# Performance work log

Measured on AMD Instinct MI355X. Metric: run time of the kernel, lower is better.

## Reference

```python
import jax, jax.numpy as jnp
import numpy as np

# Module hyperparameters (from init_kwargs)
A, B, K, P, STRIDE, PAD, ITERS = 32, 32, 3, 4, 2, 0, 3
C = P * P          # 16, input pose matrix size
D = P * P          # 16, output pose matrix size
KK = K * K         # 9
KKA = KK * A       # 288
EPS = 1e-8


def setup_inputs() -> dict:
    key = jax.random.key(0)
    k1, k2 = jax.random.split(key)
    pose = jax.random.normal(k1, (4, A * C, 32, 32), dtype=jnp.float32)
    # kaiming-uniform-like scale for W [kkA, B*D, C]
    W = jax.random.normal(k2, (KKA, B * D, C), dtype=jnp.float32) / np.sqrt(C).astype(np.float32)
    return {"pose": pose, "W": W}


def _unfold(x):
    # Equivalent of F.unfold(x, K, stride=STRIDE, padding=0), channel-major,
    # kernel positions (ki, kj) fastest -> (b, ch, KK, l)
    b, ch, h, w = x.shape
    oh = (h - K) // STRIDE + 1
    ow = (w - K) // STRIDE + 1
    hi = STRIDE * (oh - 1) + 1
    wi = STRIDE * (ow - 1) + 1
    cols = [x[:, :, i:i + hi:STRIDE, j:j + wi:STRIDE]
            for i in range(K) for j in range(K)]
    p = jnp.stack(cols, axis=2)  # (b, ch, KK, oh, ow)
    return p.reshape(b, ch, KK, oh * ow), oh, ow


def _squash(s):
    # standard capsule squash along last (pose) dim
    n2 = jnp.sum(s * s, axis=-1, keepdims=True)
    return s * n2 / ((1.0 + n2) * jnp.sqrt(n2 + EPS))


def reference(pose, W):
    b = pose.shape[0]
    p, oh, ow = _unfold(pose)               # (b, A*C, KK, l)
    l = oh * ow
    # view(b,A,C,kk,l) -> permute(0,4,3,1,2) -> (b,l,kk,A,C) -> (b,l,kkA,C)
    p = p.reshape(b, A, C, KK, l).transpose(0, 4, 3, 1, 2).reshape(b, l, KKA, C)
    # votes: W [kkA, B*D, C] @ pose [..., C, 1]
    votes = jnp.einsum('kdc,blkc->blkd', W, p).reshape(b, l, KKA, B, D)
    # routing-by-agreement
    logits = jnp.zeros((b, l, KKA, B, 1), dtype=pose.dtype)
    v = None
    for _ in range(ITERS):
        c = jax.nn.softmax(logits, axis=3)              # over B output capsules
        s = jnp.sum(c * votes, axis=2, keepdims=True)   # (b, l, 1, B, D)
        v = _squash(s)
        logits = logits + jnp.sum(v * votes, axis=-1, keepdims=True)
    v = v[:, :, 0].reshape(b, l, B * D)     # (b, l, B*D)
    v = v.transpose(0, 2, 1)                # (b, B*D, l)
    return v.reshape(b, B * D, oh, ow)
```

## Files before the change

### kernel.cpp

```cpp
#include <hip/hip_runtime.h>
#include <math.h>

#define KC   18
#define KPC  16
#define NP   928
#define NPT  29

typedef __attribute__((ext_vector_type(8)))  short short8;
typedef __attribute__((ext_vector_type(16))) float f32x16;

__device__ __forceinline__ unsigned short f2bf(float x) {
    union { float f; unsigned u; } v; v.f = x;
    unsigned r = v.u + 0x7fffu + ((v.u >> 16) & 1u);
    return (unsigned short)(r >> 16);
}
__device__ __forceinline__ float bf2f(unsigned short h) {
    union { unsigned u; float f; } v; v.u = ((unsigned)h) << 16;
    return v.f;
}

__global__ void wprep(const float* __restrict__ W,
                      unsigned short* __restrict__ Whi,
                      unsigned short* __restrict__ Wlo)
{
    int idx = (blockIdx.x * 256 + threadIdx.x) * 4;
    float4 x = *(const float4*)(W + idx);
    ushort4 h, l;
    h.x = f2bf(x.x); l.x = f2bf(x.x - bf2f(h.x));
    h.y = f2bf(x.y); l.y = f2bf(x.y - bf2f(h.y));
    h.z = f2bf(x.z); l.z = f2bf(x.z - bf2f(h.z));
    h.w = f2bf(x.w); l.w = f2bf(x.w - bf2f(h.w));
    *(ushort4*)(Whi + idx) = h;
    *(ushort4*)(Wlo + idx) = l;
}

__global__ __launch_bounds__(256) void unfold(const float* __restrict__ pose,
                                              unsigned short* __restrict__ Phi,
                                              unsigned short* __restrict__ Plo)
{
    __shared__ float lds[16 * 1057];
    const int bid = blockIdx.x;
    const int batch = bid >> 5;
    const int a = bid & 31;
    const int t = threadIdx.x;

    const float* src = pose + ((size_t)batch * 512 + a * 16) * 1024;
#pragma unroll
    for (int c = 0; c < 16; ++c) {
        float4 v = *(const float4*)(src + c * 1024 + t * 4);
        float* d = &lds[c * 1057 + (t >> 3) * 33 + (t & 7) * 4];
        d[0] = v.x; d[1] = v.y; d[2] = v.z; d[3] = v.w;
    }
    __syncthreads();

    const int c = t & 15;
    const int px = t >> 4;
    for (int it = 0; it < 15; ++it) {
        int pos = it * 16 + px;
        bool ok = pos < 225;
        int pc = ok ? pos : 224;
        int oi = pc / 15, oj = pc - oi * 15;
#pragma unroll
        for (int ki = 0; ki < 3; ++ki)
#pragma unroll
            for (int kj = 0; kj < 3; ++kj) {
                float val = lds[c * 1057 + (oi * 2 + ki) * 33 + (oj * 2 + kj)];
                unsigned short hh = f2bf(val);
                unsigned short ll = f2bf(val - bf2f(hh));
                if (ok) {
                    size_t o = ((size_t)((ki * 3 + kj) * 32 + a) * NP
                                + batch * 225 + pos) * 16 + c;
                    Phi[o] = hh;
                    Plo[o] = ll;
                }
            }
    }
}

template<int ITER>
__global__ __launch_bounds__(512, 2) void route(const unsigned short* __restrict__ Whi,
                                                const unsigned short* __restrict__ Wlo,
                                                const unsigned short* __restrict__ Phi,
                                                const unsigned short* __restrict__ Plo,
                                                const float* __restrict__ V,
                                                unsigned short* __restrict__ part)
{
    __shared__ float2 smb[2][8][32];

    const int bid = blockIdx.x;
    const int pt = bid % NPT;
    const int kc = bid / NPT;
    const int t = threadIdx.x;
    const int w = t >> 6;
    const int l = t & 63;
    const int col = l & 31;
    const int h = l >> 5;
    const int gpos = pt * 32 + col;
    const int bd0 = w * 64;

    float vf[2][16];
    if constexpr (ITER > 0) {
        const float* vp = V + (size_t)gpos * 512 + bd0 + 4 * h;
#pragma unroll
        for (int m = 0; m < 2; ++m)
#pragma unroll
            for (int q = 0; q < 4; ++q) {
                float4 x = *(const float4*)(vp + m * 32 + 8 * q);
                vf[m][q * 4 + 0] = x.x; vf[m][q * 4 + 1] = x.y;
                vf[m][q * 4 + 2] = x.z; vf[m][q * 4 + 3] = x.w;
            }
    }

    f32x16 s[2];
#pragma unroll
    for (int m = 0; m < 2; ++m)
#pragma unroll
        for (int r = 0; r < 16; ++r) s[m][r] = 0.f;

    const size_t k0 = (size_t)kc * KPC;
    const unsigned short* pWh = Whi + (k0 * 512 + bd0 + col) * 16 + 8 * h;
    const unsigned short* pWl = Wlo + (k0 * 512 + bd0 + col) * 16 + 8 * h;
    const unsigned short* pPh = Phi + (k0 * NP + gpos) * 16 + 8 * h;
    const unsigned short* pPl = Plo + (k0 * NP + gpos) * 16 + 8 * h;

    short8 ah0 = *(const short8*)(pWh);
    short8 ah1 = *(const short8*)(pWh + 512);
    short8 al0 = *(const short8*)(pWl);
    short8 al1 = *(const short8*)(pWl + 512);
    short8 bh  = *(const short8*)(pPh);
    short8 bl  = *(const short8*)(pPl);

    for (int kl = 0; kl < KPC; ++kl) {
        const int nw = (kl + 1) * 8192;
        const int np = (kl + 1) * 14848;
        short8 nah0 = *(const short8*)(pWh + nw);
        short8 nah1 = *(const short8*)(pWh + nw + 512);
        short8 nal0 = *(const short8*)(pWl + nw);
        short8 nal1 = *(const short8*)(pWl + nw + 512);
        short8 nbh  = *(const short8*)(pPh + np);
        short8 nbl  = *(const short8*)(pPl + np);

        if constexpr (ITER == 0) {
            s[0] = __builtin_amdgcn_mfma_f32_32x32x16_bf16(ah0, bh, s[0], 0, 0, 0);
            s[1] = __builtin_amdgcn_mfma_f32_32x32x16_bf16(ah1, bh, s[1], 0, 0, 0);
            s[0] = __builtin_amdgcn_mfma_f32_32x32x16_bf16(ah0, bl, s[0], 0, 0, 0);
            s[1] = __builtin_amdgcn_mfma_f32_32x32x16_bf16(ah1, bl, s[1], 0, 0, 0);
            s[0] = __builtin_amdgcn_mfma_f32_32x32x16_bf16(al0, bh, s[0], 0, 0, 0);
            s[1] = __builtin_amdgcn_mfma_f32_32x32x16_bf16(al1, bh, s[1], 0, 0, 0);
        } else {
            f32x16 v[2];
#pragma unroll
            for (int m = 0; m < 2; ++m)
#pragma unroll
                for (int r = 0; r < 16; ++r) v[m][r] = 0.f;
            v[0] = __builtin_amdgcn_mfma_f32_32x32x16_bf16(ah0, bh, v[0], 0, 0, 0);
            v[1] = __builtin_amdgcn_mfma_f32_32x32x16_bf16(ah1, bh, v[1], 0, 0, 0);
            v[0] = __builtin_amdgcn_mfma_f32_32x32x16_bf16(ah0, bl, v[0], 0, 0, 0);
            v[1] = __builtin_amdgcn_mfma_f32_32x32x16_bf16(ah1, bl, v[1], 0, 0, 0);
            v[0] = __builtin_amdgcn_mfma_f32_32x32x16_bf16(al0, bh, v[0], 0, 0, 0);
            v[1] = __builtin_amdgcn_mfma_f32_32x32x16_bf16(al1, bh, v[1], 0, 0, 0);

            float lp[4] = {0.f, 0.f, 0.f, 0.f};
#pragma unroll
            for (int m = 0; m < 2; ++m)
#pragma unroll
                for (int q = 0; q < 4; ++q)
#pragma unroll
                    for (int i = 0; i < 4; ++i)
                        lp[m * 2 + (q >> 1)] = fmaf(v[m][q * 4 + i], vf[m][q * 4 + i],
                                                    lp[m * 2 + (q >> 1)]);
#pragma unroll
            for (int j = 0; j < 4; ++j) lp[j] += __shfl_xor(lp[j], 32);

            float mw = fmaxf(fmaxf(lp[0], lp[1]), fmaxf(lp[2], lp[3]));
            float ex[4], sw = 0.f;
#pragma unroll
            for (int j = 0; j < 4; ++j) { ex[j] = __expf(lp[j] - mw); sw += ex[j]; }
            if (h == 0) smb[kl & 1][w][col] = make_float2(mw, sw);
            asm volatile("s_waitcnt lgkmcnt(0)\n\ts_barrier" ::: "memory");
            float2 z[8];
            float M = -1e30f;
#pragma unroll
            for (int ww = 0; ww < 8; ++ww) { z[ww] = smb[kl & 1][ww][col]; M = fmaxf(M, z[ww].x); }
            float denom = 0.f;
#pragma unroll
            for (int ww = 0; ww < 8; ++ww) denom += z[ww].y * __expf(z[ww].x - M);
            float scale = __expf(mw - M) / denom;
            float cw[4];
#pragma unroll
            for (int j = 0; j < 4; ++j) cw[j] = ex[j] * scale;

#pragma unroll
            for (int m = 0; m < 2; ++m)
#pragma unroll
                for (int q = 0; q < 4; ++q)
#pragma unroll
                    for (int i = 0; i < 4; ++i)
                        s[m][q * 4 + i] = fmaf(cw[m * 2 + (q >> 1)], v[m][q * 4 + i],
                                               s[m][q * 4 + i]);
        }

        ah0 = nah0; ah1 = nah1; al0 = nal0; al1 = nal1; bh = nbh; bl = nbl;
    }

    const float mult = (ITER == 0) ? (1.0f / 32.0f) : 1.0f;
#pragma unroll
    for (int m = 0; m < 2; ++m)
#pragma unroll
        for (int q = 0; q < 4; ++q)
#pragma unroll
            for (int i = 0; i < 4; ++i) {
                int bd = bd0 + m * 32 + 8 * q + 4 * h + i;
                part[((size_t)(kc * 512 + bd)) * NP + gpos] = f2bf(s[m][q * 4 + i] * mult);
            }
}

template<int ITER>
__global__ __launch_bounds__(256) void squash(const unsigned short* __restrict__ part,
                                              float* __restrict__ V,
                                              float* __restrict__ out)
{
    int bid = blockIdx.x;
    int pt = bid >> 2, bg = bid & 3;
    int t = threadIdx.x;
    int pos = pt * 32 + (t & 31);
    int b = bg * 8 + (t >> 5);

    float s[16];
#pragma unroll
    for (int d = 0; d < 16; ++d) s[d] = 0.f;
    for (int kc = 0; kc < KC; ++kc) {
        const unsigned short* pp = part + ((size_t)(kc * 512 + b * 16)) * NP + pos;
#pragma unroll
        for (int d = 0; d < 16; ++d) s[d] += bf2f(pp[(size_t)d * NP]);
    }
    float n2 = 0.f;
#pragma unroll
    for (int d = 0; d < 16; ++d) n2 = fmaf(s[d], s[d], n2);
    float scale = n2 / ((1.0f + n2) * sqrtf(n2 + 1e-8f));

    if constexpr (ITER < 2) {
        float* vp = V + (size_t)pos * 512 + b * 16;
#pragma unroll
        for (int d = 0; d < 16; ++d) {
            float val = s[d] * scale;
            if constexpr (ITER == 0) vp[d] = val;
            else                     vp[d] += val;
        }
    } else {
        if (pos < 900) {
            int batch = pos / 225;
            int opos = pos - batch * 225;
            float* op = out + ((size_t)(batch * 512 + b * 16)) * 225 + opos;
#pragma unroll
            for (int d = 0; d < 16; ++d) op[(size_t)d * 225] = s[d] * scale;
        }
    }
}

extern "C" void kernel_launch(void* const* d_in, const int* in_sizes, int n_in,
                              void* d_out, int out_size, void* d_ws, size_t ws_size,
                              hipStream_t stream)
{
    const float* pose = (const float*)d_in[0];
    const float* Wg   = (const float*)d_in[1];
    float* out = (float*)d_out;
    char* ws = (char*)d_ws;
    unsigned short* Whi  = (unsigned short*)(ws);
    unsigned short* Wlo  = (unsigned short*)(ws + 4718592);
    unsigned short* Phi  = (unsigned short*)(ws + 9437184);
    unsigned short* Plo  = (unsigned short*)(ws + 17989632);
    unsigned short* part = (unsigned short*)(ws + 26542080);
    float* V             = (float*)(ws + 43646976);

    wprep<<<2304, 256, 0, stream>>>(Wg, Whi, Wlo);
    unfold<<<128, 256, 0, stream>>>(pose, Phi, Plo);

    route<0><<<NPT * KC, 512, 0, stream>>>(Whi, Wlo, Phi, Plo, V, part);
    squash<0><<<116, 256, 0, stream>>>(part, V, out);
    route<1><<<NPT * KC, 512, 0, stream>>>(Whi, Wlo, Phi, Plo, V, part);
    squash<1><<<116, 256, 0, stream>>>(part, V, out);
    route<2><<<NPT * KC, 512, 0, stream>>>(Whi, Wlo, Phi, Plo, V, part);
    squash<2><<<116, 256, 0, stream>>>(part, V, out);
}
```

Before: 245.0 us.

## Stage W and pose tiles through double-buffered LDS with cooperative coalesced loads

Rather than each wave loading its own W and pose fragments straight from global memory with register prefetch, the block now loads each k-slice of W hi/lo and pose hi/lo cooperatively into a double-buffered LDS tile. MFMA operands are then read from LDS. The next slice is prefetched into registers and written to the other buffer before a barrier. This is meant to improve coalescing and cut redundant global traffic, since the pose fragments were read by all 8 waves. In exchange it adds about 68 KB of LDS per block, which may limit the two-blocks-per-CU occupancy target, and it adds a barrier per k step in iteration 0.

```diff
diff --git a/kernel.cpp b/kernel.cpp
--- a/kernel.cpp
+++ b/kernel.cpp
@@ -85,6 +85,8 @@
                                                 const float* __restrict__ V,
                                                 unsigned short* __restrict__ part)
 {
+    __shared__ __align__(16) unsigned short wlds[2][16384];
+    __shared__ __align__(16) unsigned short plds[2][1024];
     __shared__ float2 smb[2][8][32];
 
     const int bid = blockIdx.x;
@@ -97,6 +99,7 @@
     const int h = l >> 5;
     const int gpos = pt * 32 + col;
     const int bd0 = w * 64;
+    const int k0 = kc * KPC;
 
     float vf[2][16];
     if constexpr (ITER > 0) {
@@ -117,28 +120,43 @@
 #pragma unroll
         for (int r = 0; r < 16; ++r) s[m][r] = 0.f;
 
-    const size_t k0 = (size_t)kc * KPC;
-    const unsigned short* pWh = Whi + (k0 * 512 + bd0 + col) * 16 + 8 * h;
-    const unsigned short* pWl = Wlo + (k0 * 512 + bd0 + col) * 16 + 8 * h;
-    const unsigned short* pPh = Phi + (k0 * NP + gpos) * 16 + 8 * h;
-    const unsigned short* pPl = Plo + (k0 * NP + gpos) * 16 + 8 * h;
-
-    short8 ah0 = *(const short8*)(pWh);
-    short8 ah1 = *(const short8*)(pWh + 512);
-    short8 al0 = *(const short8*)(pWl);
-    short8 al1 = *(const short8*)(pWl + 512);
-    short8 bh  = *(const short8*)(pPh);
-    short8 bl  = *(const short8*)(pPl);
+    const unsigned short* gP = (w & 1) ? Plo : Phi;
+
+    {
+        const size_t wb = (size_t)k0 * 8192;
+        const size_t pb = ((size_t)k0 * NP + pt * 32) * 16;
+        short8 r0 = *(const short8*)(Whi + wb + t * 8);
+        short8 r1 = *(const short8*)(Whi + wb + 4096 + t * 8);
+        short8 r2 = *(const short8*)(Wlo + wb + t * 8);
+        short8 r3 = *(const short8*)(Wlo + wb + 4096 + t * 8);
+        short8 rp = *(const short8*)(gP + pb + l * 8);
+        *(short8*)&wlds[0][t * 8]          = r0;
+        *(short8*)&wlds[0][4096 + t * 8]   = r1;
+        *(short8*)&wlds[0][8192 + t * 8]   = r2;
+        *(short8*)&wlds[0][12288 + t * 8]  = r3;
+        if (w < 2) *(short8*)&plds[0][w * 512 + l * 8] = rp;
+    }
+    __syncthreads();
 
     for (int kl = 0; kl < KPC; ++kl) {
-        const int nw = (kl + 1) * 8192;
-        const int np = (kl + 1) * 14848;
-        short8 nah0 = *(const short8*)(pWh + nw);
-        short8 nah1 = *(const short8*)(pWh + nw + 512);
-        short8 nal0 = *(const short8*)(pWl + nw);
-        short8 nal1 = *(const short8*)(pWl + nw + 512);
-        short8 nbh  = *(const short8*)(pPh + np);
-        short8 nbl  = *(const short8*)(pPl + np);
+        const int cb = kl & 1, nb = cb ^ 1;
+
+        const size_t wb = (size_t)(k0 + kl + 1) * 8192;
+        const size_t pb = ((size_t)(k0 + kl + 1) * NP + pt * 32) * 16;
+        short8 r0 = *(const short8*)(Whi + wb + t * 8);
+        short8 r1 = *(const short8*)(Whi + wb + 4096 + t * 8);
+        short8 r2 = *(const short8*)(Wlo + wb + t * 8);
+        short8 r3 = *(const short8*)(Wlo + wb + 4096 + t * 8);
+        short8 rp = *(const short8*)(gP + pb + l * 8);
+
+        const int wa = (bd0 + col) * 16 + 8 * h;
+        const int pa = col * 16 + 8 * h;
+        short8 ah0 = *(const short8*)&wlds[cb][wa];
+        short8 ah1 = *(const short8*)&wlds[cb][wa + 512];
+        short8 al0 = *(const short8*)&wlds[cb][8192 + wa];
+        short8 al1 = *(const short8*)&wlds[cb][8192 + wa + 512];
+        short8 bh  = *(const short8*)&plds[cb][pa];
+        short8 bl  = *(const short8*)&plds[cb][512 + pa];
 
         if constexpr (ITER == 0) {
             s[0] = __builtin_amdgcn_mfma_f32_32x32x16_bf16(ah0, bh, s[0], 0, 0, 0);
@@ -147,6 +165,13 @@
             s[1] = __builtin_amdgcn_mfma_f32_32x32x16_bf16(ah1, bl, s[1], 0, 0, 0);
             s[0] = __builtin_amdgcn_mfma_f32_32x32x16_bf16(al0, bh, s[0], 0, 0, 0);
             s[1] = __builtin_amdgcn_mfma_f32_32x32x16_bf16(al1, bh, s[1], 0, 0, 0);
+
+            *(short8*)&wlds[nb][t * 8]         = r0;
+            *(short8*)&wlds[nb][4096 + t * 8]  = r1;
+            *(short8*)&wlds[nb][8192 + t * 8]  = r2;
+            *(short8*)&wlds[nb][12288 + t * 8] = r3;
+            if (w < 2) *(short8*)&plds[nb][w * 512 + l * 8] = rp;
+            asm volatile("s_waitcnt lgkmcnt(0)\n\ts_barrier" ::: "memory");
         } else {
             f32x16 v[2];
 #pragma unroll
@@ -176,12 +201,19 @@
             float ex[4], sw = 0.f;
 #pragma unroll
             for (int j = 0; j < 4; ++j) { ex[j] = __expf(lp[j] - mw); sw += ex[j]; }
-            if (h == 0) smb[kl & 1][w][col] = make_float2(mw, sw);
+            if (h == 0) smb[cb][w][col] = make_float2(mw, sw);
+
+            *(short8*)&wlds[nb][t * 8]         = r0;
+            *(short8*)&wlds[nb][4096 + t * 8]  = r1;
+            *(short8*)&wlds[nb][8192 + t * 8]  = r2;
+            *(short8*)&wlds[nb][12288 + t * 8] = r3;
+            if (w < 2) *(short8*)&plds[nb][w * 512 + l * 8] = rp;
             asm volatile("s_waitcnt lgkmcnt(0)\n\ts_barrier" ::: "memory");
+
             float2 z[8];
             float M = -1e30f;
 #pragma unroll
-            for (int ww = 0; ww < 8; ++ww) { z[ww] = smb[kl & 1][ww][col]; M = fmaxf(M, z[ww].x); }
+            for (int ww = 0; ww < 8; ++ww) { z[ww] = smb[cb][ww][col]; M = fmaxf(M, z[ww].x); }
             float denom = 0.f;
 #pragma unroll
             for (int ww = 0; ww < 8; ++ww) denom += z[ww].y * __expf(z[ww].x - M);
@@ -199,8 +231,6 @@
                         s[m][q * 4 + i] = fmaf(cw[m * 2 + (q >> 1)], v[m][q * 4 + i],
                                                s[m][q * 4 + i]);
         }
-
-        ah0 = nah0; ah1 = nah1; al0 = nal0; al1 = nal1; bh = nbh; bl = nbl;
     }
 
     const float mult = (ITER == 0) ? (1.0f / 32.0f) : 1.0f;
```

Measured after the change: 265.6 us. 1.08x slower.

## Rebalance k-chunk split and remap route blocks for XCD-local L2 reuse

Applied to the files above, without the earlier changes.

Changes the k split from 18 chunks of 16 to 16 chunks of 18, so route launches 464 blocks instead of 522. Block IDs are remapped so that, with round-robin dispatch over 8 XCDs, each XCD handles two k-chunks across all position tiles. That keeps each chunk's W slice resident in one XCD's L2. The smaller partial buffer shifts the V workspace offset, and squash also needs its KC loop to shrink to 16. Fewer blocks means fewer waves, at the cost of longer per-block loops.

```diff
diff --git a/kernel.cpp b/kernel.cpp
--- a/kernel.cpp
+++ b/kernel.cpp
@@ -1,8 +1,8 @@
 #include <hip/hip_runtime.h>
 #include <math.h>
 
-#define KC   18
-#define KPC  16
+#define KC   16
+#define KPC  18
 #define NP   928
 #define NPT  29
 
@@ -88,8 +88,10 @@
     __shared__ float2 smb[2][8][32];
 
     const int bid = blockIdx.x;
-    const int pt = bid % NPT;
-    const int kc = bid / NPT;
+    const int s  = bid & 7;
+    const int j  = bid >> 3;
+    const int kc = s * 2 + (j >= NPT ? 1 : 0);
+    const int pt = (j >= NPT) ? (j - NPT) : j;
     const int t = threadIdx.x;
     const int w = t >> 6;
     const int l = t & 63;
@@ -111,11 +113,11 @@
             }
     }
 
-    f32x16 s[2];
+    f32x16 s_acc[2];
 #pragma unroll
     for (int m = 0; m < 2; ++m)
 #pragma unroll
-        for (int r = 0; r < 16; ++r) s[m][r] = 0.f;
+        for (int r = 0; r < 16; ++r) s_acc[m][r] = 0.f;
 
     const size_t k0 = (size_t)kc * KPC;
     const unsigned short* pWh = Whi + (k0 * 512 + bd0 + col) * 16 + 8 * h;
@@ -141,12 +143,12 @@
         short8 nbl  = *(const short8*)(pPl + np);
 
         if constexpr (ITER == 0) {
-            s[0] = __builtin_amdgcn_mfma_f32_32x32x16_bf16(ah0, bh, s[0], 0, 0, 0);
-            s[1] = __builtin_amdgcn_mfma_f32_32x32x16_bf16(ah1, bh, s[1], 0, 0, 0);
-            s[0] = __builtin_amdgcn_mfma_f32_32x32x16_bf16(ah0, bl, s[0], 0, 0, 0);
-            s[1] = __builtin_amdgcn_mfma_f32_32x32x16_bf16(ah1, bl, s[1], 0, 0, 0);
-            s[0] = __builtin_amdgcn_mfma_f32_32x32x16_bf16(al0, bh, s[0], 0, 0, 0);
-            s[1] = __builtin_amdgcn_mfma_f32_32x32x16_bf16(al1, bh, s[1], 0, 0, 0);
+            s_acc[0] = __builtin_amdgcn_mfma_f32_32x32x16_bf16(ah0, bh, s_acc[0], 0, 0, 0);
+            s_acc[1] = __builtin_amdgcn_mfma_f32_32x32x16_bf16(ah1, bh, s_acc[1], 0, 0, 0);
+            s_acc[0] = __builtin_amdgcn_mfma_f32_32x32x16_bf16(ah0, bl, s_acc[0], 0, 0, 0);
+            s_acc[1] = __builtin_amdgcn_mfma_f32_32x32x16_bf16(ah1, bl, s_acc[1], 0, 0, 0);
+            s_acc[0] = __builtin_amdgcn_mfma_f32_32x32x16_bf16(al0, bh, s_acc[0], 0, 0, 0);
+            s_acc[1] = __builtin_amdgcn_mfma_f32_32x32x16_bf16(al1, bh, s_acc[1], 0, 0, 0);
         } else {
             f32x16 v[2];
 #pragma unroll
@@ -170,12 +172,12 @@
                         lp[m * 2 + (q >> 1)] = fmaf(v[m][q * 4 + i], vf[m][q * 4 + i],
                                                     lp[m * 2 + (q >> 1)]);
 #pragma unroll
-            for (int j = 0; j < 4; ++j) lp[j] += __shfl_xor(lp[j], 32);
+            for (int j2 = 0; j2 < 4; ++j2) lp[j2] += __shfl_xor(lp[j2], 32);
 
             float mw = fmaxf(fmaxf(lp[0], lp[1]), fmaxf(lp[2], lp[3]));
             float ex[4], sw = 0.f;
 #pragma unroll
-            for (int j = 0; j < 4; ++j) { ex[j] = __expf(lp[j] - mw); sw += ex[j]; }
+            for (int j2 = 0; j2 < 4; ++j2) { ex[j2] = __expf(lp[j2] - mw); sw += ex[j2]; }
             if (h == 0) smb[kl & 1][w][col] = make_float2(mw, sw);
             asm volatile("s_waitcnt lgkmcnt(0)\n\ts_barrier" ::: "memory");
             float2 z[8];
@@ -188,7 +190,7 @@
             float scale = __expf(mw - M) / denom;
             float cw[4];
 #pragma unroll
-            for (int j = 0; j < 4; ++j) cw[j] = ex[j] * scale;
+            for (int j2 = 0; j2 < 4; ++j2) cw[j2] = ex[j2] * scale;
 
 #pragma unroll
             for (int m = 0; m < 2; ++m)
@@ -196,8 +198,8 @@
                 for (int q = 0; q < 4; ++q)
 #pragma unroll
                     for (int i = 0; i < 4; ++i)
-                        s[m][q * 4 + i] = fmaf(cw[m * 2 + (q >> 1)], v[m][q * 4 + i],
-                                               s[m][q * 4 + i]);
+                        s_acc[m][q * 4 + i] = fmaf(cw[m * 2 + (q >> 1)], v[m][q * 4 + i],
+                                                   s_acc[m][q * 4 + i]);
         }
 
         ah0 = nah0; ah1 = nah1; al0 = nal0; al1 = nal1; bh = nbh; bl = nbl;
@@ -211,7 +213,7 @@
 #pragma unroll
             for (int i = 0; i < 4; ++i) {
                 int bd = bd0 + m * 32 + 8 * q + 4 * h + i;
-                part[((size_t)(kc * 512 + bd)) * NP + gpos] = f2bf(s[m][q * 4 + i] * mult);
+                part[((size_t)(kc * 512 + bd)) * NP + gpos] = f2bf(s_acc[m][q * 4 + i] * mult);
             }
 }
 
@@ -271,15 +273,15 @@
     unsigned short* Phi  = (unsigned short*)(ws + 9437184);
     unsigned short* Plo  = (unsigned short*)(ws + 17989632);
     unsigned short* part = (unsigned short*)(ws + 26542080);
-    float* V             = (float*)(ws + 43646976);
+    float* V             = (float*)(ws + 41746432);
 
     wprep<<<2304, 256, 0, stream>>>(Wg, Whi, Wlo);
     unfold<<<128, 256, 0, stream>>>(pose, Phi, Plo);
 
-    route<0><<<NPT * KC, 512, 0, stream>>>(Whi, Wlo, Phi, Plo, V, part);
+    route<0><<<8 * 2 * NPT, 512, 0, stream>>>(Whi, Wlo, Phi, Plo, V, part);
     squash<0><<<116, 256, 0, stream>>>(part, V, out);
-    route<1><<<NPT * KC, 512, 0, stream>>>(Whi, Wlo, Phi, Plo, V, part);
+    route<1><<<8 * 2 * NPT, 512, 0, stream>>>(Whi, Wlo, Phi, Plo, V, part);
     squash<1><<<116, 256, 0, stream>>>(part, V, out);
-    route<2><<<NPT * KC, 512, 0, stream>>>(Whi, Wlo, Phi, Plo, V, part);
+    route<2><<<8 * 2 * NPT, 512, 0, stream>>>(Whi, Wlo, Phi, Plo, V, part);
     squash<2><<<116, 256, 0, stream>>>(part, V, out);
 }
```

After: 214.5 us. -12.5%, faster.
